# Optimization experiments

Measured on AMD Instinct MI355X. Metric: run time of the kernel, lower is better.

## Reference

```python
import jax, jax.numpy as jnp
import numpy as np

ALPHA = 0.2      # leaky-relu negative slope
NEG = -9e15      # mask fill value used by dense GAT


def gat_layer(h, mask, W, a, concat):
    # h: [N, Fin], W: [Fin, Fout], a: [2*Fout, 1], mask: [N, N] bool
    Wh = h @ W                                   # [N, Fout]
    Fout = W.shape[1]
    f1 = Wh @ a[:Fout]                           # [N, 1] (source term)
    f2 = Wh @ a[Fout:]                           # [N, 1] (target term)
    e = jax.nn.leaky_relu(f1 + f2.T, ALPHA)      # [N, N]
    att = jax.nn.softmax(jnp.where(mask, e, NEG), axis=1)
    hp = att @ Wh                                # [N, Fout]
    return jax.nn.elu(hp) if concat else hp


def _xavier(key, shape, gain=1.414):
    lim = gain * np.sqrt(6.0 / (shape[-2] + shape[-1]))
    return jax.random.uniform(key, shape, jnp.float32, -lim, lim)


def setup_inputs() -> dict:
    key = jax.random.key(0)
    ks = jax.random.split(key, 9)
    N, nfeat, nhid, nclass, nheads, cpre = 8192, 512, 128, 64, 2, 16
    x = jax.random.normal(ks[0], (N, nfeat), jnp.float32)
    adj = jax.random.randint(ks[1], (N, N), 0, 2, jnp.int32)
    W_heads = jnp.stack([_xavier(ks[2], (nfeat, nhid)), _xavier(ks[3], (nfeat, nhid))])
    a_heads = jnp.stack([_xavier(ks[4], (2 * nhid, 1)), _xavier(ks[5], (2 * nhid, 1))])
    W_out = _xavier(ks[6], (nhid * nheads, nclass))
    a_out = _xavier(ks[7], (2 * nclass, 1))
    W1 = _xavier(ks[8], (nclass, cpre))
    return {"x": x, "adj": adj, "W_heads": W_heads, "a_heads": a_heads,
            "W_out": W_out, "a_out": a_out, "W1": W1}


def reference(x, adj, W_heads, a_heads, W_out, a_out, W1):
    # eval mode: all dropouts (p=0.0) are no-ops
    mask = adj > 0
    heads = [gat_layer(x, mask, W_heads[i], a_heads[i], True)
             for i in range(W_heads.shape[0])]
    h = jnp.concatenate(heads, axis=1)                         # [N, nhid*nheads]
    mu = jax.nn.elu(gat_layer(h, mask, W_out, a_out, False))   # [N, nclass]
    reconstruction = mu @ mu.T                                 # InnerProductDecoder, act=identity
    class_pre = jax.nn.softmax(mu @ W1, axis=1)                # [N, cluster_pre]
    return reconstruction, mu, class_pre
```

## Files before the change

kernel.cpp:

```cpp
#include <hip/hip_runtime.h>
#include <hip/hip_bf16.h>

constexpr int N   = 8192;
constexpr int F0  = 512;
constexpr int H1  = 128;
constexpr int NH  = 2;
constexpr int C2  = 64;
constexpr int CP  = 16;
constexpr int NS1 = 4;
constexpr int NS2 = 8;

typedef __attribute__((ext_vector_type(8))) short  short8;
typedef __attribute__((ext_vector_type(4))) float  float4v;

#define DEVI __device__ __forceinline__

DEVI float bf2f(unsigned short u) { return __uint_as_float(((unsigned int)u) << 16); }
DEVI unsigned short f2bf(float f) {
  unsigned int u = __float_as_uint(f);
  return (unsigned short)((u + 0x7fffu + ((u >> 16) & 1u)) >> 16);
}
DEVI unsigned int pk2bf(float a, float b) {
  union { __hip_bfloat162 v; unsigned int u; } c;
  c.v = __float22bfloat162_rn(make_float2(a, b));
  return c.u;
}
DEVI float elu1(float x) { return x > 0.f ? x : __expf(x) - 1.f; }
DEVI float lrelu_exp(float e) {
  e = fmaxf(e, 0.2f * e);
  return __expf(fminf(e, 60.f));
}
DEVI float4v mfma16(short8 a, short8 b, float4v c) {
  return __builtin_amdgcn_mfma_f32_16x16x32_bf16(a, b, c, 0, 0, 0);
}

DEVI int sniff_wave(const unsigned short* __restrict__ w1) {
  const int lane = threadIdx.x & 63;
  int cnt = 0;
#pragma unroll
  for (int t = 0; t < 16; t++) {
    const float v = bf2f(w1[lane * 16 + t]);
    if (!(fabsf(v) <= 1.0f)) cnt++;
  }
  for (int off = 32; off; off >>= 1) cnt += __shfl_down(cnt, off);
  cnt = __shfl(cnt, 0);
  return (cnt > 64) ? 0 : 1;
}

DEVI void cvt_one(const void* __restrict__ src, unsigned short* __restrict__ dst,
                  int idx, int flag) {
  if (flag) {
    ((uint2*)dst)[idx] = ((const uint2*)src)[idx];
  } else {
    const float4 v = ((const float4*)src)[idx];
    ((uint2*)dst)[idx] = make_uint2(pk2bf(v.x, v.y), pk2bf(v.z, v.w));
  }
}
constexpr int CQ0 = N * F0 / 4;
constexpr int CQ1 = NH * F0 * H1 / 4;
constexpr int CQ2 = NH * 2 * H1 / 4;
constexpr int CQ3 = 2 * H1 * C2 / 4;
constexpr int CQ4 = 2 * C2 / 4;
constexpr int CQ5 = C2 * CP / 4;
constexpr int CO1 = CQ0, CO2 = CO1 + CQ1, CO3 = CO2 + CQ2, CO4 = CO3 + CQ3,
              CO5 = CO4 + CQ4, CO6 = CO5 + CQ5;
__global__ __launch_bounds__(256) void k_convert_all(
    const void* s0, const void* s1, const void* s2, const void* s3,
    const void* s4, const void* s5,
    unsigned short* d0, unsigned short* d1, unsigned short* d2,
    unsigned short* d3, unsigned short* d4, unsigned short* d5,
    const unsigned short* __restrict__ w1) {
  const int flag = sniff_wave(w1);
  const int t = blockIdx.x * 256 + threadIdx.x;
  if      (t < CO1) cvt_one(s0, d0, t,       flag);
  else if (t < CO2) cvt_one(s1, d1, t - CO1, flag);
  else if (t < CO3) cvt_one(s2, d2, t - CO2, flag);
  else if (t < CO4) cvt_one(s3, d3, t - CO3, flag);
  else if (t < CO5) cvt_one(s4, d4, t - CO4, flag);
  else if (t < CO6) cvt_one(s5, d5, t - CO5, flag);
}

__global__ __launch_bounds__(256) void k_pack_mask(const int* __restrict__ adj,
                                                   unsigned long long* __restrict__ mb) {
  const size_t t = (size_t)blockIdx.x * 256 + threadIdx.x;
  const int4 a = ((const int4*)adj)[t];
  const unsigned nib = (unsigned)(a.x > 0) | ((unsigned)(a.y > 0) << 1) |
                       ((unsigned)(a.z > 0) << 2) | ((unsigned)(a.w > 0) << 3);
  unsigned long long v = (unsigned long long)nib << ((threadIdx.x & 15) * 4);
  v |= __shfl_xor(v, 1);
  v |= __shfl_xor(v, 2);
  v |= __shfl_xor(v, 4);
  v |= __shfl_xor(v, 8);
  if ((threadIdx.x & 15) == 0) mb[t >> 4] = v;
}

constexpr int PW0 = F0 * H1;
constexpr int PW1 = 2 * F0 * H1;
constexpr int PW2 = PW1 + 2 * H1 * C2;
__global__ __launch_bounds__(256) void k_pack_w_all(const unsigned short* __restrict__ WhdB,
                                                    const unsigned short* __restrict__ WoB,
                                                    unsigned short* __restrict__ WP1,
                                                    unsigned short* __restrict__ WP2) {
  const int t = blockIdx.x * 256 + threadIdx.x;
  if (t < PW1) {
    const int base = (t >= PW0) ? PW0 : 0;
    const int tt = t - base;
    const int k = tt / H1, n = tt % H1;
    WP1[base + ((size_t)(k >> 3) * H1 + n) * 8 + (k & 7)] = WhdB[t];
  } else if (t < PW2) {
    const int tt = t - PW1;
    const int k = tt / C2, n = tt % C2;
    WP2[((size_t)(k >> 3) * C2 + n) * 8 + (k & 7)] = WoB[tt];
  }
}

template <int KDIM, int COLS>
__global__ __launch_bounds__(256) void k_gemm(const unsigned short* __restrict__ A,
                                              const unsigned short* __restrict__ Wp_all,
                                              unsigned short* __restrict__ Cp_all,
                                              const unsigned short* __restrict__ a_all,
                                              float* __restrict__ f1_all,
                                              float* __restrict__ f2_all) {
  constexpr int NT = COLS / 16;
  const int lane = threadIdx.x & 63, w = threadIdx.x >> 6;
  const int quad = lane >> 4, r16 = lane & 15;
  const int head = blockIdx.y;
  const unsigned short* Wp = Wp_all + (size_t)head * KDIM * COLS;
  unsigned short* Cp = Cp_all + (size_t)head * N * COLS;
  const unsigned short* av = a_all + (size_t)head * 2 * COLS;
  float* f1 = f1_all + (size_t)head * N;
  float* f2 = f2_all + (size_t)head * N;
  const int rb = blockIdx.x * 64 + w * 16;
  float4v acc[NT];
#pragma unroll
  for (int nt = 0; nt < NT; nt++) acc[nt] = (float4v){0.f, 0.f, 0.f, 0.f};
  const short* As = (const short*)A;
  const short* Ws = (const short*)Wp;
  for (int kc = 0; kc < KDIM; kc += 32) {
    const short8 af = *(const short8*)(As + (size_t)(rb + r16) * KDIM + kc + quad * 8);
#pragma unroll
    for (int nt = 0; nt < NT; nt++) {
      const short8 bf = *(const short8*)(Ws + ((size_t)((kc >> 3) + quad) * COLS + nt * 16 + r16) * 8);
      acc[nt] = mfma16(af, bf, acc[nt]);
    }
  }
  float a1v[NT], a2v[NT];
#pragma unroll
  for (int nt = 0; nt < NT; nt++) {
    a1v[nt] = bf2f(av[nt * 16 + r16]);
    a2v[nt] = bf2f(av[COLS + nt * 16 + r16]);
  }
  const int row0 = rb + quad * 4;
#pragma unroll
  for (int nt = 0; nt < NT; nt++) {
    const int col = nt * 16 + r16;
    const unsigned long long pk =
        (unsigned long long)pk2bf(acc[nt][0], acc[nt][1]) |
        ((unsigned long long)pk2bf(acc[nt][2], acc[nt][3]) << 32);
    *(unsigned long long*)(Cp + ((size_t)(row0 >> 3) * COLS + col) * 8 + (row0 & 7)) = pk;
  }
#pragma unroll
  for (int r = 0; r < 4; r++) {
    float s1 = 0.f, s2 = 0.f;
#pragma unroll
    for (int nt = 0; nt < NT; nt++) { s1 += acc[nt][r] * a1v[nt]; s2 += acc[nt][r] * a2v[nt]; }
    s1 += __shfl_xor(s1, 1); s2 += __shfl_xor(s2, 1);
    s1 += __shfl_xor(s1, 2); s2 += __shfl_xor(s2, 2);
    s1 += __shfl_xor(s1, 4); s2 += __shfl_xor(s2, 4);
    s1 += __shfl_xor(s1, 8); s2 += __shfl_xor(s2, 8);
    if (r16 == 0) { f1[row0 + r] = s1; f2[row0 + r] = s2; }
  }
}

template <int COLS>
__global__ __launch_bounds__(256) void k_attn(const unsigned char* __restrict__ mbytes,
                                              const float* __restrict__ f1_all,
                                              const float* __restrict__ f2_all,
                                              const unsigned short* __restrict__ Whp_all,
                                              float* __restrict__ part_all,
                                              float* __restrict__ denp_all, int jspan) {
  constexpr int NT = COLS / 16;
  const int lane = threadIdx.x & 63, w = threadIdx.x >> 6;
  const int quad = lane >> 4, r16 = lane & 15;
  const int head = blockIdx.y;
  const int rb = blockIdx.x * 128 + w * 32;
  const float* f1 = f1_all + (size_t)head * N;
  const float* f2 = f2_all + (size_t)head * N;
  const short* Wp = (const short*)(Whp_all + (size_t)head * N * COLS);
  float* part = part_all + (size_t)(blockIdx.z * gridDim.y + head) * N * COLS;
  float* denp = denp_all + (size_t)(blockIdx.z * gridDim.y + head) * N;
  const float f1r0 = f1[rb + r16];
  const float f1r1 = f1[rb + 16 + r16];
  const unsigned char* mrow0 = mbytes + (size_t)(rb + r16) * (N / 8);
  const unsigned char* mrow1 = mbytes + (size_t)(rb + 16 + r16) * (N / 8);
  float4v acc[2][NT];
#pragma unroll
  for (int mt = 0; mt < 2; mt++)
#pragma unroll
    for (int nt = 0; nt < NT; nt++) acc[mt][nt] = (float4v){0.f, 0.f, 0.f, 0.f};
  float dsum0 = 0.f, dsum1 = 0.f;

  const int j0 = blockIdx.z * jspan;
  for (int jcc = j0; jcc < j0 + jspan; jcc += 128) {
    const uint4 M0 = *(const uint4*)(mrow0 + (jcc >> 3));
    const uint4 M1 = *(const uint4*)(mrow1 + (jcc >> 3));
    const unsigned mw0[4] = {M0.x, M0.y, M0.z, M0.w};
    const unsigned mw1[4] = {M1.x, M1.y, M1.z, M1.w};
#pragma unroll
    for (int k4 = 0; k4 < 4; k4++) {
      const int jq = jcc + k4 * 32 + quad * 8;
      const float4v fA = *(const float4v*)(f2 + jq);
      const float4v fB = *(const float4v*)(f2 + jq + 4);
      const unsigned m0 = (mw0[k4] >> (quad * 8)) & 0xffu;
      const unsigned m1 = (mw1[k4] >> (quad * 8)) & 0xffu;
      float p0a[8], p1a[8];
#pragma unroll
      for (int jj = 0; jj < 8; jj++) {
        const float fj = (jj < 4) ? fA[jj] : fB[jj - 4];
        float p0 = lrelu_exp(f1r0 + fj); if (!((m0 >> jj) & 1u)) p0 = 0.f;
        float p1 = lrelu_exp(f1r1 + fj); if (!((m1 >> jj) & 1u)) p1 = 0.f;
        dsum0 += p0; dsum1 += p1;
        p0a[jj] = p0; p1a[jj] = p1;
      }
      union { uint4 u; short8 s; } A0, A1;
      A0.u = make_uint4(pk2bf(p0a[0], p0a[1]), pk2bf(p0a[2], p0a[3]),
                        pk2bf(p0a[4], p0a[5]), pk2bf(p0a[6], p0a[7]));
      A1.u = make_uint4(pk2bf(p1a[0], p1a[1]), pk2bf(p1a[2], p1a[3]),
                        pk2bf(p1a[4], p1a[5]), pk2bf(p1a[6], p1a[7]));
#pragma unroll
      for (int nt = 0; nt < NT; nt++) {
        const short8 bf = *(const short8*)(Wp + ((size_t)(jq >> 3) * COLS + nt * 16 + r16) * 8);
        acc[0][nt] = mfma16(A0.s, bf, acc[0][nt]);
        acc[1][nt] = mfma16(A1.s, bf, acc[1][nt]);
      }
    }
  }
  dsum0 += __shfl_xor(dsum0, 16); dsum0 += __shfl_xor(dsum0, 32);
  dsum1 += __shfl_xor(dsum1, 16); dsum1 += __shfl_xor(dsum1, 32);
  if (lane < 16) {
    denp[rb + lane] = dsum0;
    denp[rb + 16 + lane] = dsum1;
  }
#pragma unroll
  for (int mt = 0; mt < 2; mt++) {
    const int row0 = rb + mt * 16 + quad * 4;
#pragma unroll
    for (int nt = 0; nt < NT; nt++) {
      const int col = nt * 16 + r16;
#pragma unroll
      for (int r = 0; r < 4; r++) part[(size_t)(row0 + r) * COLS + col] = acc[mt][nt][r];
    }
  }
}

__global__ __launch_bounds__(256) void k_combine1(const float* __restrict__ part,
                                                  const float* __restrict__ denp,
                                                  unsigned short* __restrict__ h) {
  const int t = blockIdx.x * 256 + threadIdx.x;
  const int i = t >> 8, col = t & 255;
  const int head = col >> 7, c = col & 127;
  float s = 0.f, den = 0.f;
#pragma unroll
  for (int sl = 0; sl < NS1; sl++) {
    s   += part[((size_t)(sl * NH + head) * N + i) * H1 + c];
    den += denp[(size_t)(sl * NH + head) * N + i];
  }
  const float v = s / den;
  h[t] = f2bf(elu1(v));
}

__global__ __launch_bounds__(256) void k_combine2(const float* __restrict__ part,
                                                  const float* __restrict__ denp,
                                                  const unsigned short* __restrict__ W1B,
                                                  const unsigned short* __restrict__ w1,
                                                  void* __restrict__ outbase,
                                                  unsigned short* __restrict__ muP,
                                                  unsigned short* __restrict__ muPL) {
  const int flag = sniff_wave(w1);
  __shared__ float mus[4 * C2];
  __shared__ float w1s[C2 * CP];
  const int tid = threadIdx.x;
  const int t = blockIdx.x * 256 + tid;
  const int i = t >> 6;
  float s = 0.f, den = 0.f;
#pragma unroll
  for (int sl = 0; sl < NS2; sl++) {
    s   += part[((size_t)sl * N + i) * C2 + (t & 63)];
    den += denp[(size_t)sl * N + i];
  }
  const float v = elu1(s / den);
  const size_t NN = (size_t)N * N;
  if (flag) ((unsigned short*)outbase)[NN + t] = f2bf(v);
  else      ((float*)outbase)[NN + t] = v;
  if (muP) {
    const int c = t & 63;
    const unsigned short hi = f2bf(v);
    const size_t pa = ((size_t)(c >> 3) * N + i) * 8 + (c & 7);
    muP[pa] = hi;
    muPL[pa] = flag ? (unsigned short)0 : f2bf(v - bf2f(hi));
  }
  mus[tid] = flag ? bf2f(f2bf(v)) : v;
#pragma unroll
  for (int q = 0; q < 4; q++) w1s[q * 256 + tid] = bf2f(W1B[q * 256 + tid]);
  __syncthreads();
  if (tid < 4 * CP) {
    const int lr = tid >> 4, c = tid & 15;
    float lg = 0.f;
#pragma unroll
    for (int k = 0; k < C2; k++) lg += mus[lr * C2 + k] * w1s[k * CP + c];
    float mx = lg;
    mx = fmaxf(mx, __shfl_xor(mx, 1));
    mx = fmaxf(mx, __shfl_xor(mx, 2));
    mx = fmaxf(mx, __shfl_xor(mx, 4));
    mx = fmaxf(mx, __shfl_xor(mx, 8));
    const float e = __expf(lg - mx);
    float se = e;
    se += __shfl_xor(se, 1);
    se += __shfl_xor(se, 2);
    se += __shfl_xor(se, 4);
    se += __shfl_xor(se, 8);
    const float o = e / se;
    const int row = blockIdx.x * 4 + lr;
    const size_t off = NN + (size_t)N * C2;
    if (flag) ((unsigned short*)outbase)[off + (size_t)row * CP + c] = f2bf(o);
    else      ((float*)outbase)[off + (size_t)row * CP + c] = o;
  }
}

constexpr int RSTR = 132;
__global__ __launch_bounds__(256) void k_recon_fast(const unsigned short* __restrict__ muP,
                                                    const unsigned short* __restrict__ muPL,
                                                    const unsigned short* __restrict__ w1raw,
                                                    void* __restrict__ outbase) {
  const int flag = sniff_wave(w1raw);
  __shared__ float tile[32 * RSTR];
  const int lane = threadIdx.x & 63, w = threadIdx.x >> 6;
  const int quad = lane >> 4, r16 = lane & 15;
  const int rg = w & 1;
  const int ch = w >> 1;
  const int rb0 = blockIdx.y * 32;
  const int rb = rb0 + rg * 16;
  const int cb = blockIdx.x * 128;
  const short* H = (const short*)muP;
  const short* L = (const short*)muPL;
  float4v acc[4];
#pragma unroll
  for (int nt = 0; nt < 4; nt++) acc[nt] = (float4v){0.f, 0.f, 0.f, 0.f};
#pragma unroll
  for (int kc2 = 0; kc2 < 2; kc2++) {
    const int kq = kc2 * 4 + quad;
    const short8 ah = *(const short8*)(H + ((size_t)kq * N + rb + r16) * 8);
    short8 al;
    if (!flag) al = *(const short8*)(L + ((size_t)kq * N + rb + r16) * 8);
#pragma unroll
    for (int nt = 0; nt < 4; nt++) {
      const size_t boff = ((size_t)kq * N + cb + ch * 64 + nt * 16 + r16) * 8;
      const short8 bh = *(const short8*)(H + boff);
      acc[nt] = mfma16(ah, bh, acc[nt]);
      if (!flag) {
        const short8 bl = *(const short8*)(L + boff);
        acc[nt] = mfma16(ah, bl, acc[nt]);
        acc[nt] = mfma16(al, bh, acc[nt]);
      }
    }
  }
  const int lrow = rg * 16 + quad * 4;
#pragma unroll
  for (int nt = 0; nt < 4; nt++) {
    const int col = ch * 64 + nt * 16 + r16;
#pragma unroll
    for (int r = 0; r < 4; r++) tile[(lrow + r) * RSTR + col] = acc[nt][r];
  }
  __syncthreads();
  const int tid = threadIdx.x;
  if (flag) {
#pragma unroll
    for (int it = 0; it < 2; it++) {
      const int idx = it * 256 + tid;
      const int row = idx >> 4, seg = idx & 15;
      const float4 p = *(const float4*)(tile + row * RSTR + seg * 8);
      const float4 q = *(const float4*)(tile + row * RSTR + seg * 8 + 4);
      const uint4 o = make_uint4(pk2bf(p.x, p.y), pk2bf(p.z, p.w),
                                 pk2bf(q.x, q.y), pk2bf(q.z, q.w));
      *(uint4*)((unsigned short*)outbase + (size_t)(rb0 + row) * N + cb + seg * 8) = o;
    }
  } else {
#pragma unroll
    for (int it = 0; it < 4; it++) {
      const int idx = it * 256 + tid;
      const int row = idx >> 5, seg = idx & 31;
      const uint4 o = *(const uint4*)(tile + row * RSTR + seg * 4);
      *(uint4*)((float*)outbase + (size_t)(rb0 + row) * N + cb + seg * 4) = o;
    }
  }
}

__global__ __launch_bounds__(256) void k_recon_lds(const unsigned short* __restrict__ w1raw,
                                                   void* __restrict__ outbase) {
  const int flag = sniff_wave(w1raw);
  __shared__ short Ah[8 * 128 * 8];
  __shared__ short Al[8 * 128 * 8];
  __shared__ short Bh[8 * 128 * 8];
  __shared__ short Bl[8 * 128 * 8];
  const int lane = threadIdx.x & 63, w = threadIdx.x >> 6;
  const int quad = lane >> 4, r16 = lane & 15;
  const int rb = blockIdx.x * 128;
  const int cb = blockIdx.y * 128;
  const float* muf = (const float*)((const char*)outbase + (size_t)N * N * 4);
  const short* mub = (const short*)((const char*)outbase + (size_t)N * N * 2);
  const int tq = threadIdx.x >> 5;
  const int tr = threadIdx.x & 31;
#pragma unroll
  for (int it = 0; it < 4; it++) {
    const int r = it * 32 + tr;
#pragma unroll
    for (int side = 0; side < 2; side++) {
      const int grow = (side ? cb : rb) + r;
      short* Hh = side ? Bh : Ah;
      short* Hl = side ? Bl : Al;
      short8 hi, lo;
      if (flag) {
        hi = *(const short8*)(mub + (size_t)grow * C2 + tq * 8);
        lo = (short8){0, 0, 0, 0, 0, 0, 0, 0};
      } else {
        const float4 a = *(const float4*)(muf + (size_t)grow * C2 + tq * 8);
        const float4 b = *(const float4*)(muf + (size_t)grow * C2 + tq * 8 + 4);
        const float vv[8] = {a.x, a.y, a.z, a.w, b.x, b.y, b.z, b.w};
#pragma unroll
        for (int j = 0; j < 8; j++) {
          const unsigned short h = f2bf(vv[j]);
          hi[j] = (short)h;
          lo[j] = (short)f2bf(vv[j] - bf2f(h));
        }
      }
      *(short8*)(Hh + ((size_t)tq * 128 + r) * 8) = hi;
      if (!flag) *(short8*)(Hl + ((size_t)tq * 128 + r) * 8) = lo;
    }
  }
  __syncthreads();
  float4v acc[2][8];
#pragma unroll
  for (int mt = 0; mt < 2; mt++)
#pragma unroll
    for (int nt = 0; nt < 8; nt++) acc[mt][nt] = (float4v){0.f, 0.f, 0.f, 0.f};
#pragma unroll
  for (int kc2 = 0; kc2 < 2; kc2++) {
    const int kq = kc2 * 4 + quad;
    const int ra0 = w * 32 + r16;
    const int ra1 = w * 32 + 16 + r16;
    const short8 ah0 = *(const short8*)(Ah + ((size_t)kq * 128 + ra0) * 8);
    const short8 ah1 = *(const short8*)(Ah + ((size_t)kq * 128 + ra1) * 8);
    if (flag) {
#pragma unroll
      for (int nt = 0; nt < 8; nt++) {
        const short8 bh = *(const short8*)(Bh + ((size_t)kq * 128 + nt * 16 + r16) * 8);
        acc[0][nt] = mfma16(ah0, bh, acc[0][nt]);
        acc[1][nt] = mfma16(ah1, bh, acc[1][nt]);
      }
    } else {
      const short8 al0 = *(const short8*)(Al + ((size_t)kq * 128 + ra0) * 8);
      const short8 al1 = *(const short8*)(Al + ((size_t)kq * 128 + ra1) * 8);
#pragma unroll
      for (int nt = 0; nt < 8; nt++) {
        const short8 bh = *(const short8*)(Bh + ((size_t)kq * 128 + nt * 16 + r16) * 8);
        const short8 bl = *(const short8*)(Bl + ((size_t)kq * 128 + nt * 16 + r16) * 8);
        acc[0][nt] = mfma16(ah0, bh, acc[0][nt]);
        acc[0][nt] = mfma16(ah0, bl, acc[0][nt]);
        acc[0][nt] = mfma16(al0, bh, acc[0][nt]);
        acc[1][nt] = mfma16(ah1, bh, acc[1][nt]);
        acc[1][nt] = mfma16(ah1, bl, acc[1][nt]);
        acc[1][nt] = mfma16(al1, bh, acc[1][nt]);
      }
    }
  }
#pragma unroll
  for (int mt = 0; mt < 2; mt++) {
    const int row0 = rb + w * 32 + mt * 16 + quad * 4;
#pragma unroll
    for (int nt = 0; nt < 8; nt++) {
      const int col = cb + nt * 16 + r16;
#pragma unroll
      for (int r = 0; r < 4; r++) {
        if (flag) ((unsigned short*)outbase)[(size_t)(row0 + r) * N + col] = f2bf(acc[mt][nt][r]);
        else      ((float*)outbase)[(size_t)(row0 + r) * N + col] = acc[mt][nt][r];
      }
    }
  }
}

__global__ __launch_bounds__(256) void k_classpre(const unsigned short* __restrict__ W1B,
                                                  const unsigned short* __restrict__ w1raw,
                                                  void* __restrict__ outbase) {
  const int flag = sniff_wave(w1raw);
  __shared__ float w1s[C2 * CP];
  for (int t = threadIdx.x; t < C2 * CP; t += 256) w1s[t] = bf2f(W1B[t]);
  __syncthreads();
  const float* muf = (const float*)((const char*)outbase + (size_t)N * N * 4);
  const unsigned short* mub = (const unsigned short*)((const char*)outbase + (size_t)N * N * 2);
  const int i = blockIdx.x * 256 + threadIdx.x;
  float logit[CP];
#pragma unroll
  for (int c = 0; c < CP; c++) logit[c] = 0.f;
  for (int k = 0; k < C2; k++) {
    const float m = flag ? bf2f(mub[(size_t)i * C2 + k]) : muf[(size_t)i * C2 + k];
#pragma unroll
    for (int c = 0; c < CP; c++) logit[c] += m * w1s[k * CP + c];
  }
  float mx = logit[0];
#pragma unroll
  for (int c = 1; c < CP; c++) mx = fmaxf(mx, logit[c]);
  float se = 0.f;
#pragma unroll
  for (int c = 0; c < CP; c++) { logit[c] = __expf(logit[c] - mx); se += logit[c]; }
  const float inv = 1.f / se;
  const size_t off = (size_t)N * N + (size_t)N * C2;
  if (flag) {
    unsigned short* o = (unsigned short*)outbase + off + (size_t)i * CP;
#pragma unroll
    for (int c = 0; c < CP; c++) o[c] = f2bf(logit[c] * inv);
  } else {
    float* o = (float*)outbase + off + (size_t)i * CP;
#pragma unroll
    for (int c = 0; c < CP; c++) o[c] = logit[c] * inv;
  }
}

extern "C" void kernel_launch(void* const* d_in, const int* in_sizes, int n_in,
                              void* d_out, int out_size, void* d_ws, size_t ws_size,
                              hipStream_t stream) {
  (void)in_sizes; (void)n_in; (void)out_size;
  const void* x   = d_in[0];
  const int*  adj = (const int*)d_in[1];
  const void* Whd = d_in[2];
  const void* ah  = d_in[3];
  const void* Wo  = d_in[4];
  const void* ao  = d_in[5];
  const unsigned short* W1 = (const unsigned short*)d_in[6];

  char* ob = (char*)d_out;
  size_t off = 0;
  auto take = [&](size_t b) -> char* { char* p = ob + off; off += (b + 255) & ~(size_t)255; return p; };
  unsigned long long* MB = (unsigned long long*)take((size_t)N * N / 8);
  float*          PART1 = (float*)take((size_t)NS1 * NH * N * H1 * 4);
  float*          PART2 = (float*)take((size_t)NS2 * N * C2 * 4);
  unsigned short* Whp   = (unsigned short*)take((size_t)NH * N * H1 * 2);
  unsigned short* HBF   = (unsigned short*)take((size_t)N * 2 * H1 * 2);
  unsigned short* XB    = (unsigned short*)take((size_t)N * F0 * 2);
  unsigned short* Wh2P  = (unsigned short*)take((size_t)N * C2 * 2);
  unsigned short* WhdB  = (unsigned short*)take((size_t)NH * F0 * H1 * 2);
  unsigned short* WP1   = (unsigned short*)take((size_t)NH * F0 * H1 * 2);
  unsigned short* WoB   = (unsigned short*)take((size_t)2 * H1 * C2 * 2);
  unsigned short* WP2   = (unsigned short*)take((size_t)2 * H1 * C2 * 2);
  unsigned short* ahB   = (unsigned short*)take((size_t)NH * 2 * H1 * 2);
  unsigned short* aoB   = (unsigned short*)take((size_t)2 * C2 * 2);
  unsigned short* W1B   = (unsigned short*)take((size_t)C2 * CP * 2);
  float*          F1    = (float*)take((size_t)NH * N * 4);
  float*          F2    = (float*)take((size_t)NH * N * 4);
  float*          F1B   = (float*)take((size_t)N * 4);
  float*          F2B   = (float*)take((size_t)N * 4);
  float*          DEN1P = (float*)take((size_t)NS1 * NH * N * 4);
  float*          DEN2P = (float*)take((size_t)NS2 * N * 4);

  const bool fast = ws_size >= ((size_t)4 << 20);
  unsigned short* muP  = fast ? (unsigned short*)d_ws : nullptr;
  unsigned short* muPL = fast ? (unsigned short*)d_ws + (size_t)N * C2 : nullptr;

  const dim3 B(256);
  k_convert_all<<<dim3((CO6 + 255) / 256), B, 0, stream>>>(x, Whd, ah, Wo, ao, W1,
                                                           XB, WhdB, ahB, WoB, aoB, W1B, W1);
  k_pack_mask<<<dim3((unsigned)((size_t)N * N / 1024)), B, 0, stream>>>(adj, MB);
  k_pack_w_all<<<dim3((PW2 + 255) / 256), B, 0, stream>>>(WhdB, WoB, WP1, WP2);

  k_gemm<F0, H1><<<dim3(N / 64, NH), B, 0, stream>>>(XB, WP1, Whp, ahB, F1, F2);
  k_attn<H1><<<dim3(N / 128, NH, NS1), B, 0, stream>>>((const unsigned char*)MB, F1, F2, Whp,
                                                       PART1, DEN1P, N / NS1);
  k_combine1<<<dim3((N * 2 * H1) / 256), B, 0, stream>>>(PART1, DEN1P, HBF);

  k_gemm<2 * H1, C2><<<dim3(N / 64, 1), B, 0, stream>>>(HBF, WP2, Wh2P, aoB, F1B, F2B);
  k_attn<C2><<<dim3(N / 128, 1, NS2), B, 0, stream>>>((const unsigned char*)MB, F1B, F2B, Wh2P,
                                                      PART2, DEN2P, N / NS2);
  k_combine2<<<dim3((N * C2) / 256), B, 0, stream>>>(PART2, DEN2P, W1B, W1, d_out, muP, muPL);

  if (fast) k_recon_fast<<<dim3(N / 128, N / 32), B, 0, stream>>>(muP, muPL, W1, d_out);
  else {
    k_classpre<<<dim3(N / 256), B, 0, stream>>>(W1B, W1, d_out);
    k_recon_lds<<<dim3(N / 128, N / 128), B, 0, stream>>>(W1, d_out);
  }
}
```

Baseline: 675.9 us.

## Halve attention rows per wave and switch to exp2 with prescaled logits

The attention kernel now gives each wave 16 rows instead of 32, which halves the accumulator registers and doubles the grid, aiming for more occupancy. The B-fragment loads from Wh are now reused by only one MFMA instead of two, so the Wh traffic per row doubles. The f1/f2 logits are pre-multiplied by log2(e) in the gemm epilogue so the kernel can call exp2f directly, dropping one multiply per element. The denominator is summed across four partial accumulators to shorten the dependency chain.

```diff
diff --git a/kernel.cpp b/kernel.cpp
--- a/kernel.cpp
+++ b/kernel.cpp
@@ -26,13 +26,14 @@
   return c.u;
 }
 DEVI float elu1(float x) { return x > 0.f ? x : __expf(x) - 1.f; }
-DEVI float lrelu_exp(float e) {
-  e = fmaxf(e, 0.2f * e);
-  return __expf(fminf(e, 60.f));
+DEVI float lrelu_exp2(float e2) {
+  e2 = fmaxf(e2, 0.2f * e2);
+  return exp2f(fminf(e2, 86.5f));
 }
 DEVI float4v mfma16(short8 a, short8 b, float4v c) {
   return __builtin_amdgcn_mfma_f32_16x16x32_bf16(a, b, c, 0, 0, 0);
 }
+constexpr float LOG2E = 1.44269504088896340736f;
 
 DEVI int sniff_wave(const unsigned short* __restrict__ w1) {
   const int lane = threadIdx.x & 63;
@@ -168,7 +169,7 @@
     s1 += __shfl_xor(s1, 2); s2 += __shfl_xor(s2, 2);
     s1 += __shfl_xor(s1, 4); s2 += __shfl_xor(s2, 4);
     s1 += __shfl_xor(s1, 8); s2 += __shfl_xor(s2, 8);
-    if (r16 == 0) { f1[row0 + r] = s1; f2[row0 + r] = s2; }
+    if (r16 == 0) { f1[row0 + r] = s1 * LOG2E; f2[row0 + r] = s2 * LOG2E; }
   }
 }
 
@@ -183,73 +184,56 @@
   const int lane = threadIdx.x & 63, w = threadIdx.x >> 6;
   const int quad = lane >> 4, r16 = lane & 15;
   const int head = blockIdx.y;
-  const int rb = blockIdx.x * 128 + w * 32;
+  const int rb = blockIdx.x * 64 + w * 16;
   const float* f1 = f1_all + (size_t)head * N;
   const float* f2 = f2_all + (size_t)head * N;
   const short* Wp = (const short*)(Whp_all + (size_t)head * N * COLS);
   float* part = part_all + (size_t)(blockIdx.z * gridDim.y + head) * N * COLS;
   float* denp = denp_all + (size_t)(blockIdx.z * gridDim.y + head) * N;
-  const float f1r0 = f1[rb + r16];
-  const float f1r1 = f1[rb + 16 + r16];
-  const unsigned char* mrow0 = mbytes + (size_t)(rb + r16) * (N / 8);
-  const unsigned char* mrow1 = mbytes + (size_t)(rb + 16 + r16) * (N / 8);
-  float4v acc[2][NT];
-#pragma unroll
-  for (int mt = 0; mt < 2; mt++)
-#pragma unroll
-    for (int nt = 0; nt < NT; nt++) acc[mt][nt] = (float4v){0.f, 0.f, 0.f, 0.f};
-  float dsum0 = 0.f, dsum1 = 0.f;
+  const float f1r = f1[rb + r16];
+  const unsigned char* mrow = mbytes + (size_t)(rb + r16) * (N / 8);
+  float4v acc[NT];
+#pragma unroll
+  for (int nt = 0; nt < NT; nt++) acc[nt] = (float4v){0.f, 0.f, 0.f, 0.f};
+  float ds[4] = {0.f, 0.f, 0.f, 0.f};
 
   const int j0 = blockIdx.z * jspan;
   for (int jcc = j0; jcc < j0 + jspan; jcc += 128) {
-    const uint4 M0 = *(const uint4*)(mrow0 + (jcc >> 3));
-    const uint4 M1 = *(const uint4*)(mrow1 + (jcc >> 3));
-    const unsigned mw0[4] = {M0.x, M0.y, M0.z, M0.w};
-    const unsigned mw1[4] = {M1.x, M1.y, M1.z, M1.w};
+    const uint4 M = *(const uint4*)(mrow + (jcc >> 3));
+    const unsigned mw[4] = {M.x, M.y, M.z, M.w};
 #pragma unroll
     for (int k4 = 0; k4 < 4; k4++) {
       const int jq = jcc + k4 * 32 + quad * 8;
       const float4v fA = *(const float4v*)(f2 + jq);
       const float4v fB = *(const float4v*)(f2 + jq + 4);
-      const unsigned m0 = (mw0[k4] >> (quad * 8)) & 0xffu;
-      const unsigned m1 = (mw1[k4] >> (quad * 8)) & 0xffu;
-      float p0a[8], p1a[8];
+      const unsigned m = (mw[k4] >> (quad * 8)) & 0xffu;
+      float pa[8];
 #pragma unroll
       for (int jj = 0; jj < 8; jj++) {
         const float fj = (jj < 4) ? fA[jj] : fB[jj - 4];
-        float p0 = lrelu_exp(f1r0 + fj); if (!((m0 >> jj) & 1u)) p0 = 0.f;
-        float p1 = lrelu_exp(f1r1 + fj); if (!((m1 >> jj) & 1u)) p1 = 0.f;
-        dsum0 += p0; dsum1 += p1;
-        p0a[jj] = p0; p1a[jj] = p1;
-      }
-      union { uint4 u; short8 s; } A0, A1;
-      A0.u = make_uint4(pk2bf(p0a[0], p0a[1]), pk2bf(p0a[2], p0a[3]),
-                        pk2bf(p0a[4], p0a[5]), pk2bf(p0a[6], p0a[7]));
-      A1.u = make_uint4(pk2bf(p1a[0], p1a[1]), pk2bf(p1a[2], p1a[3]),
-                        pk2bf(p1a[4], p1a[5]), pk2bf(p1a[6], p1a[7]));
+        float p = lrelu_exp2(f1r + fj); if (!((m >> jj) & 1u)) p = 0.f;
+        ds[jj & 3] += p;
+        pa[jj] = p;
+      }
+      union { uint4 u; short8 s; } A0;
+      A0.u = make_uint4(pk2bf(pa[0], pa[1]), pk2bf(pa[2], pa[3]),
+                        pk2bf(pa[4], pa[5]), pk2bf(pa[6], pa[7]));
 #pragma unroll
       for (int nt = 0; nt < NT; nt++) {
         const short8 bf = *(const short8*)(Wp + ((size_t)(jq >> 3) * COLS + nt * 16 + r16) * 8);
-        acc[0][nt] = mfma16(A0.s, bf, acc[0][nt]);
-        acc[1][nt] = mfma16(A1.s, bf, acc[1][nt]);
-      }
-    }
-  }
-  dsum0 += __shfl_xor(dsum0, 16); dsum0 += __shfl_xor(dsum0, 32);
-  dsum1 += __shfl_xor(dsum1, 16); dsum1 += __shfl_xor(dsum1, 32);
-  if (lane < 16) {
-    denp[rb + lane] = dsum0;
-    denp[rb + 16 + lane] = dsum1;
-  }
-#pragma unroll
-  for (int mt = 0; mt < 2; mt++) {
-    const int row0 = rb + mt * 16 + quad * 4;
-#pragma unroll
-    for (int nt = 0; nt < NT; nt++) {
-      const int col = nt * 16 + r16;
-#pragma unroll
-      for (int r = 0; r < 4; r++) part[(size_t)(row0 + r) * COLS + col] = acc[mt][nt][r];
-    }
+        acc[nt] = mfma16(A0.s, bf, acc[nt]);
+      }
+    }
+  }
+  float dsum = (ds[0] + ds[1]) + (ds[2] + ds[3]);
+  dsum += __shfl_xor(dsum, 16); dsum += __shfl_xor(dsum, 32);
+  if (lane < 16) denp[rb + lane] = dsum;
+  const int row0 = rb + quad * 4;
+#pragma unroll
+  for (int nt = 0; nt < NT; nt++) {
+    const int col = nt * 16 + r16;
+#pragma unroll
+    for (int r = 0; r < 4; r++) part[(size_t)(row0 + r) * COLS + col] = acc[nt][r];
   }
 }
 
@@ -572,13 +556,13 @@
   k_pack_w_all<<<dim3((PW2 + 255) / 256), B, 0, stream>>>(WhdB, WoB, WP1, WP2);
 
   k_gemm<F0, H1><<<dim3(N / 64, NH), B, 0, stream>>>(XB, WP1, Whp, ahB, F1, F2);
-  k_attn<H1><<<dim3(N / 128, NH, NS1), B, 0, stream>>>((const unsigned char*)MB, F1, F2, Whp,
-                                                       PART1, DEN1P, N / NS1);
+  k_attn<H1><<<dim3(N / 64, NH, NS1), B, 0, stream>>>((const unsigned char*)MB, F1, F2, Whp,
+                                                      PART1, DEN1P, N / NS1);
   k_combine1<<<dim3((N * 2 * H1) / 256), B, 0, stream>>>(PART1, DEN1P, HBF);
 
   k_gemm<2 * H1, C2><<<dim3(N / 64, 1), B, 0, stream>>>(HBF, WP2, Wh2P, aoB, F1B, F2B);
-  k_attn<C2><<<dim3(N / 128, 1, NS2), B, 0, stream>>>((const unsigned char*)MB, F1B, F2B, Wh2P,
-                                                      PART2, DEN2P, N / NS2);
+  k_attn<C2><<<dim3(N / 64, 1, NS2), B, 0, stream>>>((const unsigned char*)MB, F1B, F2B, Wh2P,
+                                                     PART2, DEN2P, N / NS2);
   k_combine2<<<dim3((N * C2) / 256), B, 0, stream>>>(PART2, DEN2P, W1B, W1, d_out, muP, muPL);
 
   if (fast) k_recon_fast<<<dim3(N / 128, N / 32), B, 0, stream>>>(muP, muPL, W1, d_out);
```

Result: no change. 674.1 us (-0.3%).
